# Kernel tuning notes

Measured on AMD Instinct MI355X. Metric: run time of the kernel, lower is better.

## Reference

```python
import jax, jax.numpy as jnp
import numpy as np
from jax import lax

N_CHANNELS = 16
FIRE_RATE = 0.5
ALIVE_THRESH = 0.1


def _perceive_kernel(n_channels):
    sx = jnp.array([[-1., 0., 1.], [-2., 0., 2.], [-1., 0., 1.]], dtype=jnp.float32) / 8.0
    sy = sx.T
    ident = jnp.outer(jnp.array([0., 1., 0.], jnp.float32), jnp.array([0., 1., 0.], jnp.float32))
    base = jnp.stack([ident, sx, sy], axis=0)            # (3,3,3)
    k = jnp.tile(base, (n_channels, 1, 1))[:, None]       # (3n,1,3,3) order: id,sx,sy per channel
    return k


def _maxpool3(a):
    # torch max_pool2d(kernel=3, stride=1, padding=1) with -inf padding
    return lax.reduce_window(a, -jnp.inf, lax.max, (1, 1, 3, 3), (1, 1, 1, 1),
                             ((0, 0), (0, 0), (1, 1), (1, 1)))


def _living(x):
    return _maxpool3(x[:, 3:4]) > ALIVE_THRESH


def setup_inputs() -> dict:
    key = jax.random.key(0)
    k1, k2, k3, k4, k5 = jax.random.split(key, 5)
    B, C, H, W = 32, N_CHANNELS, 256, 256
    HID = 128
    x = jax.random.uniform(k1, (B, C, H, W), dtype=jnp.float32)
    update_rand = jax.random.uniform(k2, (B, 1, H, W), dtype=jnp.float32)
    w1 = jax.random.normal(k3, (HID, 3 * C), dtype=jnp.float32) * 0.1
    b1 = jax.random.normal(k4, (HID,), dtype=jnp.float32) * 0.1
    w2 = jax.random.normal(k5, (C, HID), dtype=jnp.float32) * 0.1
    return {"x": x, "update_rand": update_rand, "w1": w1, "b1": b1, "w2": w2}


def reference(x, update_rand, w1, b1, w2):
    kernel = _perceive_kernel(N_CHANNELS)
    begin_living = _living(x)                                        # (B,1,H,W) bool
    # depthwise perception: groups = n_channels, 3 filters per group
    y = lax.conv_general_dilated(x, kernel, (1, 1), ((1, 1), (1, 1)),
                                 feature_group_count=N_CHANNELS,
                                 dimension_numbers=("NCHW", "OIHW", "NCHW"))  # (B,3C,H,W)
    h = jax.nn.relu(jnp.einsum("bchw,oc->bohw", y, w1) + b1[None, :, None, None])
    dx = jnp.einsum("bhij,oh->boij", h, w2)                          # (B,C,H,W)
    update = (update_rand <= FIRE_RATE).astype(x.dtype)              # (B,1,H,W)
    x_new = x + dx * update
    alive = begin_living & _living(x_new)
    return x_new * alive.astype(x.dtype)
```

## Files before the change

kernel.cpp:

```cpp
#include <hip/hip_runtime.h>

#define CN 16
#define HN 128
#define IMH 256
#define IMW 256
#define HW (IMH * IMW)

typedef __attribute__((ext_vector_type(8))) short short8;
typedef __attribute__((ext_vector_type(4))) float float4v;
typedef __attribute__((ext_vector_type(2))) unsigned int uint2v;
typedef __attribute__((ext_vector_type(4))) unsigned int uint4v;

__device__ __forceinline__ unsigned int f2bf(float f) {
    unsigned int u = __builtin_bit_cast(unsigned int, f);
    u += 0x7FFFu + ((u >> 16) & 1u);
    return u >> 16;
}
__device__ __forceinline__ unsigned int pack2(float a, float b) {
    unsigned int r;
    asm("v_cvt_pk_bf16_f32 %0, %1, %2" : "=v"(r) : "v"(a), "v"(b));
    return r;
}

__global__ void nca_prep(const float* __restrict__ w1, const float* __restrict__ b1,
                         const float* __restrict__ w2,
                         unsigned short* __restrict__ a1f, unsigned short* __restrict__ b2f)
{
    int t = blockIdx.x * 256 + threadIdx.x;
    if (t < 8192) {
        int j = t & 7, lane = (t >> 3) & 63, ks = (t >> 9) & 1, mi = t >> 10;
        int hid = 16 * mi + (lane & 15);
        int k = 32 * ks + 8 * (lane >> 4) + j;
        float v = 0.f;
        if (k < 48) v = w1[hid * 48 + k];
        else if (k == 48) v = b1[hid];
        a1f[t] = (unsigned short)f2bf(v);
    }
    if (t < 2048) {
        int j = t & 7, lane = (t >> 3) & 63, ks = t >> 9;
        b2f[t] = (unsigned short)f2bf(w2[(lane & 15) * HN + 32 * ks + 8 * (lane >> 4) + j]);
    }
}

__global__ __launch_bounds__(256, 4) void nca_mfma(
    const float* __restrict__ x, const float* __restrict__ upd,
    const unsigned short* __restrict__ a1f, const unsigned short* __restrict__ b2f,
    float* __restrict__ out, float* __restrict__ xn3, unsigned char* __restrict__ bm)
{
    __shared__ __align__(16) union {
        float sx[6][16][34];
        unsigned short hb[4][16][128];
    } u;
    __shared__ __align__(16) unsigned short ybuf[128][64];
    __shared__ __align__(16) float ubuf[128];

    const int b   = blockIdx.z;
    const int i0  = blockIdx.y * 4;
    const int j0  = blockIdx.x * 32;
    const int tid = threadIdx.x;
    const int lane = tid & 63, w = tid >> 6;
    const int l15 = lane & 15, q = lane >> 4;
    const float* xb = x + (size_t)b * CN * HW;
    const float* ub = upd + (size_t)b * HW;

    short8 a1[8][2];
#pragma unroll
    for (int mi = 0; mi < 8; ++mi)
#pragma unroll
        for (int ks = 0; ks < 2; ++ks)
            a1[mi][ks] = *(const short8*)(a1f + ((mi * 2 + ks) * 64 + lane) * 8);
    short8 b2[4];
#pragma unroll
    for (int ks = 0; ks < 4; ++ks)
        b2[ks] = *(const short8*)(b2f + (ks * 64 + lane) * 8);

    const bool interior = (blockIdx.y > 0) & (blockIdx.y < 63) & (blockIdx.x > 0) & (blockIdx.x < 7);
    {
        const int col = tid & 31;
        if (interior) {
            const float* src = xb + (i0 - 1) * IMW + (j0 - 1);
#pragma unroll
            for (int rt = tid >> 5; rt < 96; rt += 8)
                u.sx[rt >> 4][rt & 15][col] = src[(rt & 15) * HW + (rt >> 4) * IMW + col];
            if (tid < 192) {
                int rt = tid >> 1, col2 = 32 + (tid & 1);
                u.sx[rt >> 4][rt & 15][col2] = src[(rt & 15) * HW + (rt >> 4) * IMW + col2];
            }
        } else {
#pragma unroll
            for (int rt = tid >> 5; rt < 96; rt += 8) {
                int rr = rt >> 4, c = rt & 15;
                int gi = i0 + rr - 1, gj = j0 + col - 1;
                float v = 0.f;
                if ((unsigned)gi < IMH && (unsigned)gj < IMW) v = xb[c * HW + gi * IMW + gj];
                u.sx[rr][c][col] = v;
            }
            if (tid < 192) {
                int rt = tid >> 1, col2 = 32 + (tid & 1);
                int rr = rt >> 4, c = rt & 15;
                int gi = i0 + rr - 1, gj = j0 + col2 - 1;
                float v = 0.f;
                if ((unsigned)gi < IMH && (unsigned)gj < IMW) v = xb[c * HW + gi * IMW + gj];
                u.sx[rr][c][col2] = v;
            }
        }
        if (tid < 128) ubuf[tid] = ub[(i0 + (tid >> 5)) * IMW + j0 + (tid & 31)];
    }
    __syncthreads();

    const int pix = tid & 127;
    const int ty  = pix >> 5, tx = pix & 31;
    const int cb  = (tid >> 7) << 3;
    float v[24];
#pragma unroll
    for (int c8 = 0; c8 < 8; ++c8) {
        const int c = cb + c8;
        float a00 = u.sx[ty][c][tx],     a01 = u.sx[ty][c][tx + 1],     a02 = u.sx[ty][c][tx + 2];
        float a10 = u.sx[ty + 1][c][tx], a11 = u.sx[ty + 1][c][tx + 1], a12 = u.sx[ty + 1][c][tx + 2];
        float a20 = u.sx[ty + 2][c][tx], a21 = u.sx[ty + 2][c][tx + 1], a22 = u.sx[ty + 2][c][tx + 2];
        v[3 * c8]     = a11;
        v[3 * c8 + 1] = ((a02 - a00) + 2.f * (a12 - a10) + (a22 - a20)) * 0.125f;
        v[3 * c8 + 2] = ((a20 - a00) + 2.f * (a21 - a01) + (a22 - a02)) * 0.125f;
        if (cb == 0 && c8 == 3) {
            float m0 = fmaxf(fmaxf(fmaxf(a00, a01), fmaxf(a02, a10)),
                             fmaxf(fmaxf(a11, a12), fmaxf(fmaxf(a20, a21), a22)));
            bm[(size_t)b * HW + (i0 + ty) * IMW + (j0 + tx)] = (m0 > 0.1f) ? 1 : 0;
        }
    }
    {
        unsigned int* yrow = (unsigned int*)&ybuf[pix][0];
        const int gbase = (cb >> 3) * 3;
        const int sw = pix & 7;
#pragma unroll
        for (int t = 0; t < 3; ++t) {
            uint4v g;
#pragma unroll
            for (int k = 0; k < 4; ++k) g[k] = pack2(v[8 * t + 2 * k], v[8 * t + 2 * k + 1]);
            *(uint4v*)&yrow[((gbase + t) ^ sw) << 2] = g;
        }
        if (cb == 8) {
            uint4v g6 = {0x3F80u, 0u, 0u, 0u};
            uint4v g7 = {};
            *(uint4v*)&yrow[(6 ^ sw) << 2] = g6;
            *(uint4v*)&yrow[(7 ^ sw) << 2] = g7;
        }
    }
    __syncthreads();

    float* ob = out + (size_t)b * CN * HW;
    float* n3 = xn3 + (size_t)b * HW;
#pragma unroll
    for (int half = 0; half < 2; ++half) {
        const int nt  = 2 * w + half;
        const int row = 16 * nt + l15;
        const unsigned short* yr = &ybuf[row][0];
        const int rsw = row & 7;
        short8 y0 = *(const short8*)(yr + ((q ^ rsw) << 3));
        short8 y1 = *(const short8*)(yr + (((4 + q) ^ rsw) << 3));
        const int hsw = l15 & 7;
#pragma unroll
        for (int mi = 0; mi < 8; ++mi) {
            float4v acc = {};
            acc = __builtin_amdgcn_mfma_f32_16x16x32_bf16(a1[mi][0], y0, acc, 0, 0, 0);
            acc = __builtin_amdgcn_mfma_f32_16x16x32_bf16(a1[mi][1], y1, acc, 0, 0, 0);
            uint2v hp;
            hp[0] = pack2(fmaxf(acc[0], 0.f), fmaxf(acc[1], 0.f));
            hp[1] = pack2(fmaxf(acc[2], 0.f), fmaxf(acc[3], 0.f));
            *(uint2v*)&u.hb[w][l15][(((2 * mi + (q >> 1)) ^ hsw) << 3) + ((q & 1) << 2)] = hp;
        }
        float4v acc2 = {};
#pragma unroll
        for (int ks = 0; ks < 4; ++ks) {
            short8 hf = *(const short8*)&u.hb[w][l15][((4 * ks + q) ^ hsw) << 3];
            acc2 = __builtin_amdgcn_mfma_f32_16x16x32_bf16(hf, b2[ks], acc2, 0, 0, 0);
        }
        const int i  = i0 + (nt >> 1);
        const int jb = j0 + ((nt & 1) << 4) + (q << 2);
        float4v xc4 = *(const float4v*)(xb + (size_t)l15 * HW + i * IMW + jb);
        float4v u4  = *(const float4v*)&ubuf[16 * nt + (q << 2)];
        float4v o;
#pragma unroll
        for (int r = 0; r < 4; ++r)
            o[r] = fmaf(acc2[r], (u4[r] <= 0.5f) ? 1.f : 0.f, xc4[r]);
        *(float4v*)(ob + l15 * HW + i * IMW + jb) = o;
        if (l15 == 3) *(float4v*)(n3 + i * IMW + jb) = o;
    }
}

__global__ __launch_bounds__(256) void nca_pass2(
    const float* __restrict__ xn3, const unsigned char* __restrict__ bm,
    float* __restrict__ out)
{
    __shared__ float s[10][264];
    const int b   = blockIdx.z;
    const int i0  = blockIdx.y * 8;
    const int tid = threadIdx.x;
    const float* n3 = xn3 + (size_t)b * HW;

#pragma unroll
    for (int t = 0; t < 3; ++t) {
        const int idx = tid + 256 * t;
        if (idx < 640) {
            const int r = idx >> 6, c4 = idx & 63;
            const int gi = i0 + r - 1;
            float4v vv;
            if ((unsigned)gi < IMH) vv = *(const float4v*)(n3 + gi * IMW + 4 * c4);
            else { vv[0] = vv[1] = vv[2] = vv[3] = -1e30f; }
            *(float4v*)&s[r][4 + 4 * c4] = vv;
        }
    }
    if (tid < 20) { const int r = tid >> 1; s[r][(tid & 1) ? 260 : 3] = -1e30f; }
    __syncthreads();

    const int c = tid;
    const unsigned char* bmb = bm + (size_t)b * HW + i0 * IMW + c;
    float* ob = out + (size_t)b * CN * HW;
#pragma unroll
    for (int r = 0; r < 8; ++r) {
        float m = fmaxf(fmaxf(fmaxf(s[r][c + 3], s[r][c + 4]), fmaxf(s[r][c + 5], s[r + 1][c + 3])),
                        fmaxf(fmaxf(s[r + 1][c + 4], s[r + 1][c + 5]),
                              fmaxf(fmaxf(s[r + 2][c + 3], s[r + 2][c + 4]), s[r + 2][c + 5])));
        if (!((m > 0.1f) && bmb[r * IMW])) {
            const int i = i0 + r;
#pragma unroll
            for (int ch = 0; ch < CN; ++ch)
                ob[ch * HW + i * IMW + c] = 0.f;
        }
    }
}

extern "C" void kernel_launch(void* const* d_in, const int* in_sizes, int n_in,
                              void* d_out, int out_size, void* d_ws, size_t ws_size,
                              hipStream_t stream) {
    const float* x   = (const float*)d_in[0];
    const float* upd = (const float*)d_in[1];
    const float* w1  = (const float*)d_in[2];
    const float* b1  = (const float*)d_in[3];
    const float* w2  = (const float*)d_in[4];
    float* out = (float*)d_out;

    char* ws = (char*)d_ws;
    float* xn3          = (float*)ws;
    unsigned char* bmp  = (unsigned char*)(ws + (8u << 20));
    unsigned short* a1f = (unsigned short*)(ws + (10u << 20));
    unsigned short* b2f = a1f + 8192;

    nca_prep<<<32, 256, 0, stream>>>(w1, b1, w2, a1f, b2f);
    nca_mfma<<<dim3(8, 64, 32), 256, 0, stream>>>(x, upd, a1f, b2f, out, xn3, bmp);
    nca_pass2<<<dim3(1, 32, 32), 256, 0, stream>>>(xn3, bmp, out);
}
```

Baseline: 418.9 us.

## Restructure perception so each thread handles four pixels and two channels

```diff
diff --git a/kernel.cpp b/kernel.cpp
--- a/kernel.cpp
+++ b/kernel.cpp
@@ -30,10 +30,10 @@
     if (t < 8192) {
         int j = t & 7, lane = (t >> 3) & 63, ks = (t >> 9) & 1, mi = t >> 10;
         int hid = 16 * mi + (lane & 15);
-        int k = 32 * ks + 8 * (lane >> 4) + j;
+        int cp = 4 * ks + (lane >> 4);
         float v = 0.f;
-        if (k < 48) v = w1[hid * 48 + k];
-        else if (k == 48) v = b1[hid];
+        if (j < 6) v = w1[hid * 48 + 6 * cp + j];
+        else if (cp == 0 && j == 6) v = b1[hid];
         a1f[t] = (unsigned short)f2bf(v);
     }
     if (t < 2048) {
@@ -48,11 +48,11 @@
     float* __restrict__ out, float* __restrict__ xn3, unsigned char* __restrict__ bm)
 {
     __shared__ __align__(16) union {
-        float sx[6][16][34];
+        float sx[6][16][36];
         unsigned short hb[4][16][128];
     } u;
     __shared__ __align__(16) unsigned short ybuf[128][64];
-    __shared__ __align__(16) float ubuf[128];
+    __shared__ __align__(16) float xcT[16][128];
 
     const int b   = blockIdx.z;
     const int i0  = blockIdx.y * 4;
@@ -104,45 +104,98 @@
                 u.sx[rr][c][col2] = v;
             }
         }
-        if (tid < 128) ubuf[tid] = ub[(i0 + (tid >> 5)) * IMW + j0 + (tid & 31)];
     }
     __syncthreads();
 
-    const int pix = tid & 127;
-    const int ty  = pix >> 5, tx = pix & 31;
-    const int cb  = (tid >> 7) << 3;
-    float v[24];
-#pragma unroll
-    for (int c8 = 0; c8 < 8; ++c8) {
-        const int c = cb + c8;
-        float a00 = u.sx[ty][c][tx],     a01 = u.sx[ty][c][tx + 1],     a02 = u.sx[ty][c][tx + 2];
-        float a10 = u.sx[ty + 1][c][tx], a11 = u.sx[ty + 1][c][tx + 1], a12 = u.sx[ty + 1][c][tx + 2];
-        float a20 = u.sx[ty + 2][c][tx], a21 = u.sx[ty + 2][c][tx + 1], a22 = u.sx[ty + 2][c][tx + 2];
-        v[3 * c8]     = a11;
-        v[3 * c8 + 1] = ((a02 - a00) + 2.f * (a12 - a10) + (a22 - a20)) * 0.125f;
-        v[3 * c8 + 2] = ((a20 - a00) + 2.f * (a21 - a01) + (a22 - a02)) * 0.125f;
-        if (cb == 0 && c8 == 3) {
-            float m0 = fmaxf(fmaxf(fmaxf(a00, a01), fmaxf(a02, a10)),
-                             fmaxf(fmaxf(a11, a12), fmaxf(fmaxf(a20, a21), a22)));
-            bm[(size_t)b * HW + (i0 + ty) * IMW + (j0 + tx)] = (m0 > 0.1f) ? 1 : 0;
-        }
-    }
+    const int qd  = tid & 31;
+    const int cp  = tid >> 5;
+    const int ty  = qd >> 3, tx4 = (qd & 7) << 2;
+
+    unsigned int w0p[4], w1p[4], w2p[4];
+    float4v cen0v, cen1v;
     {
-        unsigned int* yrow = (unsigned int*)&ybuf[pix][0];
-        const int gbase = (cb >> 3) * 3;
-        const int sw = pix & 7;
-#pragma unroll
-        for (int t = 0; t < 3; ++t) {
-            uint4v g;
-#pragma unroll
-            for (int k = 0; k < 4; ++k) g[k] = pack2(v[8 * t + 2 * k], v[8 * t + 2 * k + 1]);
-            *(uint4v*)&yrow[((gbase + t) ^ sw) << 2] = g;
-        }
-        if (cb == 8) {
-            uint4v g6 = {0x3F80u, 0u, 0u, 0u};
-            uint4v g7 = {};
-            *(uint4v*)&yrow[(6 ^ sw) << 2] = g6;
-            *(uint4v*)&yrow[(7 ^ sw) << 2] = g7;
+        const int c = 2 * cp;
+        float4v r0a = *(const float4v*)&u.sx[ty][c][tx4];
+        float4v r0b = *(const float4v*)&u.sx[ty][c][tx4 + 4];
+        float4v r1a = *(const float4v*)&u.sx[ty + 1][c][tx4];
+        float4v r1b = *(const float4v*)&u.sx[ty + 1][c][tx4 + 4];
+        float4v r2a = *(const float4v*)&u.sx[ty + 2][c][tx4];
+        float4v r2b = *(const float4v*)&u.sx[ty + 2][c][tx4 + 4];
+        float S[6], D[6];
+#pragma unroll
+        for (int j = 0; j < 6; ++j) {
+            float a0 = (j < 4) ? r0a[j] : r0b[j - 4];
+            float a1v = (j < 4) ? r1a[j] : r1b[j - 4];
+            float a2 = (j < 4) ? r2a[j] : r2b[j - 4];
+            S[j] = fmaf(2.f, a1v, a0) + a2;
+            D[j] = a2 - a0;
+        }
+        float sy0[4];
+#pragma unroll
+        for (int r = 0; r < 4; ++r) {
+            float cen = (r + 1 < 4) ? r1a[r + 1] : r1b[r - 3];
+            float sxv = (S[r + 2] - S[r]) * 0.125f;
+            sy0[r] = (fmaf(2.f, D[r + 1], D[r]) + D[r + 2]) * 0.125f;
+            w0p[r] = pack2(cen, sxv);
+            cen0v[r] = cen;
+        }
+#pragma unroll
+        for (int r = 0; r < 4; ++r) w1p[r] = __builtin_bit_cast(unsigned int, sy0[r]);
+    }
+    {
+        const int c = 2 * cp + 1;
+        float4v r0a = *(const float4v*)&u.sx[ty][c][tx4];
+        float4v r0b = *(const float4v*)&u.sx[ty][c][tx4 + 4];
+        float4v r1a = *(const float4v*)&u.sx[ty + 1][c][tx4];
+        float4v r1b = *(const float4v*)&u.sx[ty + 1][c][tx4 + 4];
+        float4v r2a = *(const float4v*)&u.sx[ty + 2][c][tx4];
+        float4v r2b = *(const float4v*)&u.sx[ty + 2][c][tx4 + 4];
+        float S[6], D[6];
+#pragma unroll
+        for (int j = 0; j < 6; ++j) {
+            float a0 = (j < 4) ? r0a[j] : r0b[j - 4];
+            float a1v = (j < 4) ? r1a[j] : r1b[j - 4];
+            float a2 = (j < 4) ? r2a[j] : r2b[j - 4];
+            S[j] = fmaf(2.f, a1v, a0) + a2;
+            D[j] = a2 - a0;
+        }
+#pragma unroll
+        for (int r = 0; r < 4; ++r) {
+            float cen = (r + 1 < 4) ? r1a[r + 1] : r1b[r - 3];
+            float sxv = (S[r + 2] - S[r]) * 0.125f;
+            float syv = (fmaf(2.f, D[r + 1], D[r]) + D[r + 2]) * 0.125f;
+            float sy0 = __builtin_bit_cast(float, w1p[r]);
+            w1p[r] = pack2(sy0, cen);
+            w2p[r] = pack2(sxv, syv);
+            cen1v[r] = cen;
+        }
+        if (cp == 1) {
+            unsigned int bits = 0;
+#pragma unroll
+            for (int r = 0; r < 4; ++r) {
+                float m0 = -1.f;
+#pragma unroll
+                for (int j = 0; j < 3; ++j) {
+                    float a0 = (r + j < 4) ? r0a[r + j] : r0b[r + j - 4];
+                    float a1v = (r + j < 4) ? r1a[r + j] : r1b[r + j - 4];
+                    float a2 = (r + j < 4) ? r2a[r + j] : r2b[r + j - 4];
+                    m0 = fmaxf(m0, fmaxf(a0, fmaxf(a1v, a2)));
+                }
+                bits |= (m0 > 0.1f ? 1u : 0u) << (8 * r);
+            }
+            *(unsigned int*)(bm + (size_t)b * HW + (i0 + ty) * IMW + j0 + tx4) = bits;
+        }
+    }
+    *(float4v*)&xcT[2 * cp][(4 * qd) ^ (((2 * cp) & 7) << 2)] = cen0v;
+    *(float4v*)&xcT[2 * cp + 1][(4 * qd) ^ (((2 * cp + 1) & 7) << 2)] = cen1v;
+    {
+        const unsigned int u3 = (cp == 0) ? 0x3F80u : 0u;
+#pragma unroll
+        for (int r = 0; r < 4; ++r) {
+            const int p = 4 * qd + r;
+            const int sw = p & 7;
+            uint4v g = {w0p[r], w1p[r], w2p[r], u3};
+            *(uint4v*)&((unsigned int*)&ybuf[p][0])[(cp ^ sw) << 2] = g;
         }
     }
     __syncthreads();
@@ -151,7 +204,7 @@
     float* n3 = xn3 + (size_t)b * HW;
 #pragma unroll
     for (int half = 0; half < 2; ++half) {
-        const int nt  = 2 * w + half;
+        const int nt  = w + 4 * half;
         const int row = 16 * nt + l15;
         const unsigned short* yr = &ybuf[row][0];
         const int rsw = row & 7;
@@ -176,8 +229,8 @@
         }
         const int i  = i0 + (nt >> 1);
         const int jb = j0 + ((nt & 1) << 4) + (q << 2);
-        float4v xc4 = *(const float4v*)(xb + (size_t)l15 * HW + i * IMW + jb);
-        float4v u4  = *(const float4v*)&ubuf[16 * nt + (q << 2)];
+        float4v xc4 = *(const float4v*)&xcT[l15][(16 * nt + 4 * q) ^ ((l15 & 7) << 2)];
+        float4v u4  = *(const float4v*)(ub + i * IMW + jb);
         float4v o;
 #pragma unroll
         for (int r = 0; r < 4; ++r)
```

Result: faster. 410.4 us (-2.0%).
